# Kernel optimization log

Measured on AMD Instinct MI355X. Metric: run time of the kernel, lower is better.

The kernel has to match this reference:

```python
import jax, jax.numpy as jnp
import numpy as np

N, M, E = 128, 256, 64
S, B = 1024, 512


def setup_inputs() -> dict:
    key = jax.random.key(0)
    ks = jax.random.split(key, 8)
    context = jax.random.normal(ks[0], (S, B, N), dtype=jnp.float32)
    z = jax.random.normal(ks[1], (M, B), dtype=jnp.float32)
    noise = jax.random.normal(ks[2], (N, B), dtype=jnp.float32)
    # parameters (match torch init semantics)
    conv_w = jax.random.normal(ks[3], (N, N, 2), dtype=jnp.float32) * (1.0 / np.sqrt(N * 2))
    conv_b = jnp.zeros((N,), dtype=jnp.float32)
    D = jnp.zeros((N, M), dtype=jnp.float32).at[:, :N].set(jnp.eye(N, dtype=jnp.float32))
    sigma = jnp.ones((N,), dtype=jnp.float32) * 0.05
    temp1 = jnp.array([0.1], dtype=jnp.float32)
    temp2 = jnp.array([0.1], dtype=jnp.float32)
    W1 = jax.random.normal(ks[4], (E, M + N), dtype=jnp.float32) * (1.0 / np.sqrt(M + N))
    b1 = jnp.zeros((E,), dtype=jnp.float32)
    W2 = jax.random.normal(ks[5], (E, E), dtype=jnp.float32) * (1.0 / np.sqrt(E))
    b2 = jnp.zeros((E,), dtype=jnp.float32)
    return {"context": context, "z": z, "noise": noise, "conv_w": conv_w,
            "conv_b": conv_b, "D": D, "sigma": sigma, "temp1": temp1,
            "W1": W1, "b1": b1, "W2": W2, "b2": b2, "temp2": temp2}


def reference(context, z, noise, conv_w, conv_b, D, sigma, temp1, W1, b1, W2, b2, temp2):
    # z_obs = D @ detach(z)  -> [N, B]
    z_obs = D @ jax.lax.stop_gradient(z)
    z_current = z_obs + sigma[:, None] * noise            # [N, B]
    z_current_t = z_current.T                             # [B, N]
    # L1 distance attention over the first S-1 frames
    distances = jnp.sum(jnp.abs(context[:-1] - z_current_t[None]), axis=2)  # [S-1, B]
    attn = jax.nn.softmax(-distances / jnp.abs(temp1[0]), axis=0)           # [S-1, B]
    # conv1d over seq axis: x [B, N, S], w [N_out, N_in, 2], valid padding -> [B, N, S-1]
    x = jnp.transpose(context, (1, 2, 0))
    enc = jax.lax.conv_general_dilated(x, conv_w, window_strides=(1,), padding='VALID',
                                       dimension_numbers=('NCH', 'OIH', 'NCH'))
    enc = enc + conv_b[None, :, None]
    encoded = jnp.transpose(enc, (2, 0, 1))               # [S-1, B, N]
    # attention-weighted sum over frames
    embedding = jnp.einsum('sbn,sb->nb', encoded, attn)   # [N, B]
    combined_t = jnp.concatenate([embedding, z], axis=0).T  # [B, N+M]
    h = jax.nn.relu(combined_t @ W1.T + b1)
    mlp_out = h @ W2.T + b2                               # [B, E]
    w_exp = jax.nn.softmax(-mlp_out.T / jnp.abs(temp2[0]), axis=0)  # [E, B]
    return w_exp
```

## Files before the change

### kernel.cpp

```cpp
#include <hip/hip_runtime.h>
#include <math.h>

#define Bq 512
#define Nq 128
#define Mq 256
#define Eq 64
#define SM1 1023
#define LOG2E 1.4426950408889634f

__device__ __forceinline__ float waveReduceSumAll(float x) {
    x += __int_as_float(__builtin_amdgcn_update_dpp(0, __float_as_int(x), 0x111, 0xf, 0xf, true));
    x += __int_as_float(__builtin_amdgcn_update_dpp(0, __float_as_int(x), 0x112, 0xf, 0xf, true));
    x += __int_as_float(__builtin_amdgcn_update_dpp(0, __float_as_int(x), 0x114, 0xf, 0xf, true));
    x += __int_as_float(__builtin_amdgcn_update_dpp(0, __float_as_int(x), 0x118, 0xf, 0xf, true));
    x += __int_as_float(__builtin_amdgcn_update_dpp(0, __float_as_int(x), 0x142, 0xf, 0xf, true));
    x += __int_as_float(__builtin_amdgcn_update_dpp(0, __float_as_int(x), 0x143, 0xf, 0xf, true));
    return __int_as_float(__builtin_amdgcn_readlane(__float_as_int(x), 63));
}

extern "C" __global__ void __launch_bounds__(512, 4)
gating_kernel(const float* __restrict__ context,
              const float* __restrict__ z,
              const float* __restrict__ noise,
              const float* __restrict__ conv_w,
              const float* __restrict__ conv_b,
              const float* __restrict__ D,
              const float* __restrict__ sigma,
              const float* __restrict__ temp1,
              const float* __restrict__ W1,
              const float* __restrict__ b1,
              const float* __restrict__ W2,
              const float* __restrict__ b2,
              const float* __restrict__ temp2,
              float* __restrict__ out)
{
    const int b    = blockIdx.x;
    const int tid  = threadIdx.x;
    const int wave = tid >> 6;
    const int lane = tid & 63;

    __shared__ __align__(16) float sA0[8][128];
    __shared__ __align__(16) float sA1[8][128];
    __shared__ float smx[8];
    __shared__ float sZ[8];
    __shared__ __align__(16) float gA0[128];
    __shared__ __align__(16) float gA1[128];
    __shared__ __align__(16) float semb[128];
    __shared__ __align__(16) float szc[128];
    __shared__ __align__(16) float szcol[256];
    __shared__ __align__(16) float shb[64];

    if (tid < 256) szcol[tid] = z[tid * Bq + b];
    __syncthreads();
    if (tid < 128) {
        const float4* Drow = (const float4*)(D + tid * Mq);
        float acc0 = 0.f, acc1 = 0.f, acc2 = 0.f, acc3 = 0.f;
        #pragma unroll 8
        for (int i = 0; i < 64; ++i) {
            float4 dv = Drow[i];
            acc0 = fmaf(dv.x, szcol[4 * i + 0], acc0);
            acc1 = fmaf(dv.y, szcol[4 * i + 1], acc1);
            acc2 = fmaf(dv.z, szcol[4 * i + 2], acc2);
            acc3 = fmaf(dv.w, szcol[4 * i + 3], acc3);
        }
        szc[tid] = (acc0 + acc1) + (acc2 + acc3) + sigma[tid] * noise[tid * Bq + b];
    }
    __syncthreads();

    const float invt = LOG2E / fabsf(temp1[0]);
    const float zcx = szc[2 * lane];
    const float zcy = szc[2 * lane + 1];

    const int lo = wave * 128;
    const int hi = min(SM1, lo + 128);
    const size_t rowstride = (size_t)Bq * Nq;
    const float* p = context + (size_t)b * Nq + 2 * lane;

    float mrun = -INFINITY, Zrun = 0.f, wprev = 0.f;
    float a0x = 0.f, a0y = 0.f, a1x = 0.f, a1y = 0.f;

    float2 cb0 = *(const float2*)(p + (size_t)lo * rowstride);
    float2 cb1 = *(const float2*)(p + (size_t)(lo + 1) * rowstride);

    for (int r = lo; r <= hi; ++r) {
        float2 c = cb0;
        cb0 = cb1;
        if (r + 2 <= hi)
            cb1 = *(const float2*)(p + (size_t)(r + 2) * rowstride);
        if (r > lo) {
            a1x = fmaf(wprev, c.x, a1x);
            a1y = fmaf(wprev, c.y, a1y);
        }
        if (r < hi) {
            float d = fabsf(c.x - zcx) + fabsf(c.y - zcy);
            d = waveReduceSumAll(d);
            float v = -d * invt;
            float w;
            if (v > mrun) {
                float sc = exp2f(mrun - v);
                Zrun *= sc; a0x *= sc; a0y *= sc; a1x *= sc; a1y *= sc; wprev *= sc;
                mrun = v; w = 1.f;
            } else {
                w = exp2f(v - mrun);
            }
            Zrun += w;
            a0x = fmaf(w, c.x, a0x);
            a0y = fmaf(w, c.y, a0y);
            wprev = w;
        }
    }

    *(float2*)&sA0[wave][2 * lane] = make_float2(a0x, a0y);
    *(float2*)&sA1[wave][2 * lane] = make_float2(a1x, a1y);
    if (lane == 0) { smx[wave] = mrun; sZ[wave] = Zrun; }
    __syncthreads();

    float gm = smx[0];
    #pragma unroll
    for (int k = 1; k < 8; ++k) gm = fmaxf(gm, smx[k]);
    float scl[8];
    float Gz = 0.f;
    #pragma unroll
    for (int k = 0; k < 8; ++k) { scl[k] = exp2f(smx[k] - gm); Gz = fmaf(scl[k], sZ[k], Gz); }

    if (tid < 128) {
        float acc = 0.f;
        #pragma unroll
        for (int k = 0; k < 8; ++k) acc = fmaf(scl[k], sA0[k][tid], acc);
        gA0[tid] = acc;
    } else if (tid < 256) {
        const int t = tid - 128;
        float acc = 0.f;
        #pragma unroll
        for (int k = 0; k < 8; ++k) acc = fmaf(scl[k], sA1[k][t], acc);
        gA1[t] = acc;
    }
    __syncthreads();

    if (tid < 128) {
        const float4* wr = (const float4*)(conv_w + tid * 256);
        float acc = 0.f;
        #pragma unroll 8
        for (int i = 0; i < 64; ++i) {
            float4 w4 = wr[i];
            acc = fmaf(w4.x, gA0[2 * i], acc);
            acc = fmaf(w4.y, gA1[2 * i], acc);
            acc = fmaf(w4.z, gA0[2 * i + 1], acc);
            acc = fmaf(w4.w, gA1[2 * i + 1], acc);
        }
        semb[tid] = acc / Gz + conv_b[tid];
    }
    __syncthreads();

    if (tid < 64) {
        const float* w1r = W1 + tid * (Nq + Mq);
        float acc = b1[tid];
        #pragma unroll 8
        for (int i = 0; i < 128; ++i) acc = fmaf(w1r[i], semb[i], acc);
        #pragma unroll 8
        for (int i = 0; i < 256; ++i) acc = fmaf(w1r[128 + i], szcol[i], acc);
        shb[tid] = fmaxf(acc, 0.f);
    }
    __syncthreads();

    if (tid < 64) {
        const float* w2r = W2 + tid * Eq;
        float acc = b2[tid];
        #pragma unroll 8
        for (int j = 0; j < 64; ++j) acc = fmaf(w2r[j], shb[j], acc);
        float v = -acc * (LOG2E / fabsf(temp2[0]));
        float mx = v;
        #pragma unroll
        for (int off = 32; off > 0; off >>= 1) mx = fmaxf(mx, __shfl_xor(mx, off, 64));
        float w = exp2f(v - mx);
        float s = w;
        #pragma unroll
        for (int off = 32; off > 0; off >>= 1) s += __shfl_xor(s, off, 64);
        out[tid * Bq + b] = w / s;
    }
}

extern "C" void kernel_launch(void* const* d_in, const int* in_sizes, int n_in,
                              void* d_out, int out_size, void* d_ws, size_t ws_size,
                              hipStream_t stream) {
    const float* context = (const float*)d_in[0];
    const float* z       = (const float*)d_in[1];
    const float* noise   = (const float*)d_in[2];
    const float* conv_w  = (const float*)d_in[3];
    const float* conv_b  = (const float*)d_in[4];
    const float* D       = (const float*)d_in[5];
    const float* sigma   = (const float*)d_in[6];
    const float* temp1   = (const float*)d_in[7];
    const float* W1      = (const float*)d_in[8];
    const float* b1      = (const float*)d_in[9];
    const float* W2      = (const float*)d_in[10];
    const float* b2      = (const float*)d_in[11];
    const float* temp2   = (const float*)d_in[12];
    float* out = (float*)d_out;

    gating_kernel<<<dim3(Bq), dim3(512), 0, stream>>>(
        context, z, noise, conv_w, conv_b, D, sigma, temp1,
        W1, b1, W2, b2, temp2, out);
}
```

Baseline: 81.01 us.

## Deepen context prefetch to 8-row ring and make online softmax branchless

Replaces the two-row register prefetch with an 8-entry register ring buffer. Its first loads are issued before the z/D prologue, so the context fetches overlap that setup work. The streaming loop is unrolled by 8 and the data-dependent max-rescale branch becomes a branchless fmax/exp2 update. The conv's second tap now takes the next row straight from the ring instead of carrying a delayed weight. The goal is to hide global-memory latency on the bandwidth-bound context stream, at the cost of more registers and an extra exp2 per row.

```diff
diff --git a/kernel.cpp b/kernel.cpp
--- a/kernel.cpp
+++ b/kernel.cpp
@@ -17,6 +17,25 @@
     x += __int_as_float(__builtin_amdgcn_update_dpp(0, __float_as_int(x), 0x143, 0xf, 0xf, true));
     return __int_as_float(__builtin_amdgcn_readlane(__float_as_int(x), 63));
 }
+
+#define ROW_BODY(K, RK, DOLOAD)                                          \
+    {                                                                    \
+        float2 c  = buf[(K)];                                            \
+        float2 cn = buf[((K) + 1) & 7];                                  \
+        if (DOLOAD) buf[(K)] = p2[(size_t)min((RK) + 8, hi) * 32768];    \
+        float d = fabsf(c.x - zcx) + fabsf(c.y - zcy);                   \
+        d = waveReduceSumAll(d);                                         \
+        float v = d * negt;                    \
+        float mnew = fmaxf(mrun, v);                                     \
+        float sc = exp2f(mrun - mnew);           \
+        float w  = exp2f(v - mnew);                                      \
+        mrun = mnew;                                                     \
+        Zrun = fmaf(Zrun, sc, w);                                        \
+        a0x = fmaf(a0x, sc, w * c.x);                                    \
+        a0y = fmaf(a0y, sc, w * c.y);                                    \
+        a1x = fmaf(a1x, sc, w * cn.x);                                   \
+        a1y = fmaf(a1y, sc, w * cn.y);                                   \
+    }
 
 extern "C" __global__ void __launch_bounds__(512, 4)
 gating_kernel(const float* __restrict__ context,
@@ -50,6 +69,15 @@
     __shared__ __align__(16) float szcol[256];
     __shared__ __align__(16) float shb[64];
 
+    const int lo = wave * 128;
+    const int hi = min(SM1, lo + 128);
+    const float2* p2 = (const float2*)context + (size_t)b * 64 + lane;
+
+    float2 buf[8];
+    #pragma unroll
+    for (int j = 0; j < 8; ++j)
+        buf[j] = p2[(size_t)min(lo + j, hi) * 32768];
+
     if (tid < 256) szcol[tid] = z[tid * Bq + b];
     __syncthreads();
     if (tid < 128) {
@@ -67,47 +95,23 @@
     }
     __syncthreads();
 
-    const float invt = LOG2E / fabsf(temp1[0]);
+    const float negt = -LOG2E / fabsf(temp1[0]);
     const float zcx = szc[2 * lane];
     const float zcy = szc[2 * lane + 1];
 
-    const int lo = wave * 128;
-    const int hi = min(SM1, lo + 128);
-    const size_t rowstride = (size_t)Bq * Nq;
-    const float* p = context + (size_t)b * Nq + 2 * lane;
-
-    float mrun = -INFINITY, Zrun = 0.f, wprev = 0.f;
+    float mrun = -INFINITY, Zrun = 0.f;
     float a0x = 0.f, a0y = 0.f, a1x = 0.f, a1y = 0.f;
 
-    float2 cb0 = *(const float2*)(p + (size_t)lo * rowstride);
-    float2 cb1 = *(const float2*)(p + (size_t)(lo + 1) * rowstride);
-
-    for (int r = lo; r <= hi; ++r) {
-        float2 c = cb0;
-        cb0 = cb1;
-        if (r + 2 <= hi)
-            cb1 = *(const float2*)(p + (size_t)(r + 2) * rowstride);
-        if (r > lo) {
-            a1x = fmaf(wprev, c.x, a1x);
-            a1y = fmaf(wprev, c.y, a1y);
-        }
-        if (r < hi) {
-            float d = fabsf(c.x - zcx) + fabsf(c.y - zcy);
-            d = waveReduceSumAll(d);
-            float v = -d * invt;
-            float w;
-            if (v > mrun) {
-                float sc = exp2f(mrun - v);
-                Zrun *= sc; a0x *= sc; a0y *= sc; a1x *= sc; a1y *= sc; wprev *= sc;
-                mrun = v; w = 1.f;
-            } else {
-                w = exp2f(v - mrun);
-            }
-            Zrun += w;
-            a0x = fmaf(w, c.x, a0x);
-            a0y = fmaf(w, c.y, a0y);
-            wprev = w;
-        }
+    int r = lo;
+    for (; r + 8 <= hi; r += 8) {
+        #pragma unroll
+        for (int k = 0; k < 8; ++k)
+            ROW_BODY(k, r + k, 1)
+    }
+    #pragma unroll
+    for (int j = 0; j < 7; ++j) {
+        if (r + j < hi)
+            ROW_BODY(j, r + j, 0)
     }
 
     *(float2*)&sA0[wave][2 * lane] = make_float2(a0x, a0y);
```

New measurement: 69.87 us. -13.8%, faster.
